# Kernel tuning notes

Measured on AMD Instinct MI355X. Metric: run time of the kernel, lower is better.

## Reference

```python
import jax, jax.numpy as jnp
import numpy as np

N = 100000
E = 1000000
IN_C, HID, OUT_C = 128, 128, 40
DROPOUT_P = 0.5
BN_EPS = 1e-5


def setup_inputs() -> dict:
    key = jax.random.key(0)
    ks = jax.random.split(key, 10)
    x = jax.random.normal(ks[0], (N, IN_C), dtype=jnp.float32)
    edge_index = jax.random.randint(ks[1], (2, E), 0, N, dtype=jnp.int32)

    def glorot(k, fan_in, fan_out):
        lim = np.sqrt(6.0 / (fan_in + fan_out)).astype(np.float32)
        return jax.random.uniform(k, (fan_in, fan_out), jnp.float32, -lim, lim)

    return {
        "x": x,
        "edge_index": edge_index,
        "W1": glorot(ks[2], IN_C, HID), "b1": jnp.zeros((HID,), jnp.float32),
        "g1": jnp.ones((HID,), jnp.float32), "be1": jnp.zeros((HID,), jnp.float32),
        "W2": glorot(ks[3], HID, HID), "b2": jnp.zeros((HID,), jnp.float32),
        "g2": jnp.ones((HID,), jnp.float32), "be2": jnp.zeros((HID,), jnp.float32),
        "W3": glorot(ks[4], HID, OUT_C), "b3": jnp.zeros((OUT_C,), jnp.float32),
    }


def _deg_inv_sqrt(dst):
    # degree from destination nodes, +1 for the added self loop (PyG gcn_norm)
    deg = jax.ops.segment_sum(jnp.ones((E,), jnp.float32), dst, num_segments=N) + 1.0
    return jax.lax.rsqrt(deg)


def _gcn_conv(h, W, b, src, dst, dinv):
    # h: [N, Cin] -> [N, Cout]; y = D^-1/2 (A + I) D^-1/2 (h W) + b
    hw = h @ W
    norm = dinv[src] * dinv[dst]                      # [E]
    msg = hw[src] * norm[:, None]                     # [E, Cout] gather (memory-bound)
    agg = jax.ops.segment_sum(msg, dst, num_segments=N)
    agg = agg + hw * (dinv * dinv)[:, None]           # self-loop contribution
    return agg + b


def _batchnorm(h, gamma, beta):
    mu = jnp.mean(h, axis=0)
    var = jnp.mean(jnp.square(h - mu), axis=0)        # biased, training mode
    return (h - mu) * jax.lax.rsqrt(var + BN_EPS) * gamma + beta


def _dropout(h, key):
    keep = jax.random.bernoulli(key, 1.0 - DROPOUT_P, h.shape)
    return jnp.where(keep, h / (1.0 - DROPOUT_P), 0.0)


def reference(x, edge_index, W1, b1, g1, be1, W2, b2, g2, be2, W3, b3):
    src, dst = edge_index[0], edge_index[1]
    dinv = _deg_inv_sqrt(dst)
    dk = jax.random.split(jax.random.key(42), 2)

    h = _gcn_conv(x, W1, b1, src, dst, dinv)
    h = _dropout(jax.nn.relu(_batchnorm(h, g1, be1)), dk[0])

    h = _gcn_conv(h, W2, b2, src, dst, dinv)
    h = _dropout(jax.nn.relu(_batchnorm(h, g2, be2)), dk[1])

    h = _gcn_conv(h, W3, b3, src, dst, dinv)
    return jax.nn.log_softmax(h, axis=1)
```

## Files before the change

kernel.cpp:

```cpp
#include <hip/hip_runtime.h>
#include <math.h>

typedef __attribute__((ext_vector_type(8))) short bf16x8;
typedef __attribute__((ext_vector_type(4))) float f32x4;

__device__ __forceinline__ float bfbits2f(unsigned short b){
  return __uint_as_float(((unsigned)b) << 16);
}
__device__ __forceinline__ unsigned short f2bfbits(float f){
  unsigned u = __float_as_uint(f);
  unsigned r = u + 0x7fffu + ((u >> 16) & 1u);
  return (unsigned short)(r >> 16);
}

__host__ __device__ __forceinline__ unsigned rotl32(unsigned v, int d){
  return (v << d) | (v >> (32 - d));
}
__host__ __device__ __forceinline__ void tf2x32(unsigned k0, unsigned k1,
                                                unsigned c0, unsigned c1,
                                                unsigned &o0, unsigned &o1)
{
  unsigned ks2 = k0 ^ k1 ^ 0x1BD11BDAu;
  unsigned x0 = c0 + k0, x1 = c1 + k1;
#define TFR(r) x0 += x1; x1 = rotl32(x1, r); x1 ^= x0;
  TFR(13) TFR(15) TFR(26) TFR(6)
  x0 += k1;  x1 += ks2 + 1u;
  TFR(17) TFR(29) TFR(16) TFR(24)
  x0 += ks2; x1 += k0 + 2u;
  TFR(13) TFR(15) TFR(26) TFR(6)
  x0 += k0;  x1 += k1 + 3u;
  TFR(17) TFR(29) TFR(16) TFR(24)
  x0 += k1;  x1 += ks2 + 4u;
  TFR(13) TFR(15) TFR(26) TFR(6)
  x0 += ks2; x1 += k0 + 5u;
#undef TFR
  o0 = x0; o1 = x1;
}

__device__ __forceinline__ void gen_mask(unsigned* __restrict__ mask,
                                         unsigned mk0, unsigned mk1,
                                         int g, int total, int M)
{
  for (int wi = g; wi < M; wi += total){
    unsigned bits = 0u;
    #pragma unroll 4
    for (int j = 0; j < 32; j++){
      unsigned w0, w1;
      tf2x32(mk0, mk1, 0u, (unsigned)wi * 32u + (unsigned)j, w0, w1);
      bits |= (((w0 ^ w1) >> 31) << j);
    }
    mask[wi] = bits;
  }
}

__global__ __launch_bounds__(256) void k_countpos(const int* __restrict__ dst,
                                                  int* __restrict__ cnt,
                                                  int* __restrict__ pos, int E)
{
  int g = blockIdx.x * 256 + threadIdx.x;
  int base = g * 4;
  if (base + 3 < E){
    int4 d = ((const int4*)dst)[g];
    int4 p;
    p.x = atomicAdd(&cnt[d.x], 1);
    p.y = atomicAdd(&cnt[d.y], 1);
    p.z = atomicAdd(&cnt[d.z], 1);
    p.w = atomicAdd(&cnt[d.w], 1);
    ((int4*)pos)[g] = p;
  } else {
    for (int j = 0; j < 4; j++){
      int e = base + j;
      if (e < E) pos[e] = atomicAdd(&cnt[dst[e]], 1);
    }
  }
}

__global__ __launch_bounds__(256) void k_blocksum(const int* __restrict__ cnt,
                                                  int* __restrict__ bsum, int N)
{
  __shared__ int sh[256];
  int t = threadIdx.x;
  int base = blockIdx.x * 1024 + t * 4;
  int s = 0;
  #pragma unroll
  for (int j = 0; j < 4; j++){ int i = base + j; if (i < N) s += cnt[i]; }
  sh[t] = s; __syncthreads();
  for (int off = 128; off; off >>= 1){
    if (t < off) sh[t] += sh[t + off];
    __syncthreads();
  }
  if (t == 0) bsum[blockIdx.x] = sh[0];
}

__global__ __launch_bounds__(256) void k_scansums(const int* __restrict__ bsum,
                                                  int* __restrict__ boff,
                                                  int* __restrict__ rowstart,
                                                  int NB, int N)
{
  __shared__ int sh[256];
  int t = threadIdx.x;
  int v = (t < NB) ? bsum[t] : 0;
  sh[t] = v; __syncthreads();
  for (int off = 1; off < 256; off <<= 1){
    int x = sh[t];
    int y = (t >= off) ? sh[t - off] : 0;
    __syncthreads();
    sh[t] = x + y;
    __syncthreads();
  }
  if (t < NB) boff[t] = sh[t] - v;
  if (t == NB - 1) rowstart[N] = sh[t];
}

__global__ __launch_bounds__(256) void k_scanfinal(const int* __restrict__ cnt,
                                                   const int* __restrict__ boff,
                                                   int* __restrict__ rowstart,
                                                   float* __restrict__ dinv, int N)
{
  __shared__ int sh[256];
  int t = threadIdx.x;
  int base = blockIdx.x * 1024 + t * 4;
  int c0 = 0, c1 = 0, c2 = 0, c3 = 0;
  if (base + 0 < N) c0 = cnt[base + 0];
  if (base + 1 < N) c1 = cnt[base + 1];
  if (base + 2 < N) c2 = cnt[base + 2];
  if (base + 3 < N) c3 = cnt[base + 3];
  int s = c0 + c1 + c2 + c3;
  sh[t] = s; __syncthreads();
  for (int off = 1; off < 256; off <<= 1){
    int x = sh[t];
    int y = (t >= off) ? sh[t - off] : 0;
    __syncthreads();
    sh[t] = x + y;
    __syncthreads();
  }
  int excl = sh[t] - s + boff[blockIdx.x];
  if (base + 0 < N){ rowstart[base+0] = excl;          dinv[base+0] = rsqrtf((float)c0 + 1.f); }
  if (base + 1 < N){ rowstart[base+1] = excl+c0;       dinv[base+1] = rsqrtf((float)c1 + 1.f); }
  if (base + 2 < N){ rowstart[base+2] = excl+c0+c1;    dinv[base+2] = rsqrtf((float)c2 + 1.f); }
  if (base + 3 < N){ rowstart[base+3] = excl+c0+c1+c2; dinv[base+3] = rsqrtf((float)c3 + 1.f); }
}

__global__ __launch_bounds__(256) void k_fill(const int* __restrict__ src,
                                              const int* __restrict__ dst,
                                              const int* __restrict__ pos,
                                              const int* __restrict__ rowstart,
                                              int* __restrict__ csr, int E)
{
  int g = blockIdx.x * 256 + threadIdx.x;
  int base = g * 4;
  if (base + 3 < E){
    int4 d = ((const int4*)dst)[g];
    int4 p = ((const int4*)pos)[g];
    int4 s = ((const int4*)src)[g];
    int r0 = rowstart[d.x], r1 = rowstart[d.y], r2 = rowstart[d.z], r3 = rowstart[d.w];
    csr[r0 + p.x] = s.x;
    csr[r1 + p.y] = s.y;
    csr[r2 + p.z] = s.z;
    csr[r3 + p.w] = s.w;
  } else {
    for (int j = 0; j < 4; j++){
      int e = base + j;
      if (e < E) csr[rowstart[dst[e]] + pos[e]] = src[e];
    }
  }
}

__global__ __launch_bounds__(256) void k_wt(const float* __restrict__ W1,
                                            const float* __restrict__ W2,
                                            const float* __restrict__ W3,
                                            unsigned short* __restrict__ WT1,
                                            unsigned short* __restrict__ WT2,
                                            unsigned short* __restrict__ WT3)
{
  const float* W; unsigned short* WT; int Cout, Cpad;
  if (blockIdx.x == 0){ W = W1; WT = WT1; Cout = 128; Cpad = 128; }
  else if (blockIdx.x == 1){ W = W2; WT = WT2; Cout = 128; Cpad = 128; }
  else { W = W3; WT = WT3; Cout = 40; Cpad = 48; }
  int tot = Cpad * 128;
  for (int i = threadIdx.x; i < tot; i += 256){
    int n = i >> 7, k = i & 127;
    float v = (n < Cout) ? W[k * Cout + n] : 0.f;
    WT[i] = f2bfbits(v);
  }
}

template<int NT, int MODE>
__global__ __launch_bounds__(256) void k_gemm_mfma(const void* __restrict__ Ap,
                                                   const unsigned short* __restrict__ WT,
                                                   const float* __restrict__ dinv,
                                                   const float* __restrict__ stats,
                                                   const float* __restrict__ g,
                                                   const float* __restrict__ be,
                                                   const unsigned* __restrict__ mask,
                                                   float invN,
                                                   unsigned short* __restrict__ outb,
                                                   int N, int Cout)
{
  __shared__ uint4 Wl4[NT * 16 * 16];
  __shared__ uint4 Al4[64 * 16];
  __shared__ float bnS[128], bnB[128];
  const int t = threadIdx.x;
  const int w = t >> 6, l = t & 63;
  const long rb0 = (long)blockIdx.x * 64;
  const int wrow0 = w * 16;

  uint4 rawU[4];
  float4 rawF[4][2];
  unsigned mword[4];
  int rr[4], cc[4];
  bool inr[4];
  #pragma unroll
  for (int i = 0; i < 4; i++){
    int idx = i * 64 + l;
    int r = idx >> 4, c = idx & 15;
    long grow = rb0 + wrow0 + r;
    rr[i] = r; cc[i] = c; inr[i] = (grow < N);
    if (inr[i]){
      if (MODE == 0){
        const float* ap = (const float*)Ap + grow * 128 + c * 8;
        rawF[i][0] = *(const float4*)ap;
        rawF[i][1] = *(const float4*)(ap + 4);
      } else {
        rawU[i] = *(const uint4*)((const unsigned short*)Ap + grow * 128 + c * 8);
        mword[i] = mask[((unsigned)grow << 2) + (c >> 2)];
      }
    }
  }

  {
    const uint4* s4 = (const uint4*)WT;
    const int tot = NT * 16 * 16;
    for (int i = t; i < tot; i += 256){
      int n = i >> 4, c = i & 15;
      Wl4[n * 16 + (c ^ (n & 15))] = s4[i];
    }
  }
  if (MODE == 2 && t < 128){
    float ss = 0.f, qq = 0.f;
    #pragma unroll
    for (int i = 0; i < 16; i++){
      ss += stats[i * 256 + t];
      qq += stats[i * 256 + 128 + t];
    }
    float mean = ss * invN;
    float var = fmaxf(qq * invN - mean * mean, 0.f);
    float rstd = rsqrtf(var + 1e-5f);
    float sc = g[t] * rstd;
    bnS[t] = sc;
    bnB[t] = be[t] - mean * sc;
  }
  __syncthreads();

  #pragma unroll
  for (int i = 0; i < 4; i++){
    uint4 chunk = make_uint4(0u, 0u, 0u, 0u);
    if (inr[i]){
      if (MODE == 0){
        chunk.x = (unsigned)f2bfbits(rawF[i][0].x) | ((unsigned)f2bfbits(rawF[i][0].y) << 16);
        chunk.y = (unsigned)f2bfbits(rawF[i][0].z) | ((unsigned)f2bfbits(rawF[i][0].w) << 16);
        chunk.z = (unsigned)f2bfbits(rawF[i][1].x) | ((unsigned)f2bfbits(rawF[i][1].y) << 16);
        chunk.w = (unsigned)f2bfbits(rawF[i][1].z) | ((unsigned)f2bfbits(rawF[i][1].w) << 16);
      } else {
        unsigned mb = mword[i] >> ((cc[i] & 3) * 8);
        const unsigned* rw = &rawU[i].x;
        unsigned* cw = &chunk.x;
        #pragma unroll
        for (int h = 0; h < 4; h++){
          int ch = cc[i] * 8 + 2 * h;
          float f0 = bfbits2f((unsigned short)(rw[h] & 0xffffu));
          float f1 = bfbits2f((unsigned short)(rw[h] >> 16));
          f0 = fmaxf(fmaf(f0, bnS[ch],     bnB[ch]),     0.f);
          f1 = fmaxf(fmaf(f1, bnS[ch + 1], bnB[ch + 1]), 0.f);
          f0 = ((mb >> (2 * h))     & 1u) ? 0.f : f0 * 2.f;
          f1 = ((mb >> (2 * h + 1)) & 1u) ? 0.f : f1 * 2.f;
          cw[h] = (unsigned)f2bfbits(f0) | ((unsigned)f2bfbits(f1) << 16);
        }
      }
    }
    Al4[(wrow0 + rr[i]) * 16 + (cc[i] ^ rr[i])] = chunk;
  }

  const int lm = l & 15, q = l >> 4;

  f32x4 acc[NT];
  #pragma unroll
  for (int nt = 0; nt < NT; nt++){
    acc[nt][0] = 0.f; acc[nt][1] = 0.f; acc[nt][2] = 0.f; acc[nt][3] = 0.f;
  }

  #pragma unroll
  for (int kt = 0; kt < 4; kt++){
    const int x = kt * 4 + q;
    bf16x8 a = *(const bf16x8*)&Al4[(wrow0 + lm) * 16 + (x ^ lm)];
    #pragma unroll
    for (int nt = 0; nt < NT; nt++){
      int brow = nt * 16 + lm;
      bf16x8 b = *(const bf16x8*)&Wl4[brow * 16 + (x ^ (brow & 15))];
      acc[nt] = __builtin_amdgcn_mfma_f32_16x16x32_bf16(a, b, acc[nt], 0, 0, 0);
    }
  }

  #pragma unroll
  for (int r = 0; r < 4; r++){
    long row = rb0 + wrow0 + q * 4 + r;
    if (row < N){
      float dv = dinv[row];
      #pragma unroll
      for (int nt = 0; nt < NT; nt++){
        int col = nt * 16 + lm;
        if (col < Cout)
          outb[row * Cout + col] = f2bfbits(acc[nt][r] * dv);
      }
    }
  }
}

#define ACC8(U) do{ uint4 _u = (U); \
  a0 += bfbits2f((unsigned short)(_u.x & 0xffffu)); \
  a1 += bfbits2f((unsigned short)(_u.x >> 16)); \
  a2 += bfbits2f((unsigned short)(_u.y & 0xffffu)); \
  a3 += bfbits2f((unsigned short)(_u.y >> 16)); \
  a4 += bfbits2f((unsigned short)(_u.z & 0xffffu)); \
  a5 += bfbits2f((unsigned short)(_u.z >> 16)); \
  a6 += bfbits2f((unsigned short)(_u.w & 0xffffu)); \
  a7 += bfbits2f((unsigned short)(_u.w >> 16)); }while(0)

__global__ __launch_bounds__(256) void k_agg128s(const unsigned short* __restrict__ hw,
                                                 const int* __restrict__ rs,
                                                 const int* __restrict__ csr,
                                                 const float* __restrict__ dinv,
                                                 unsigned short* __restrict__ outb,
                                                 float* __restrict__ stats,
                                                 unsigned* __restrict__ mask,
                                                 unsigned mk0, unsigned mk1, int M,
                                                 int N)
{
  const int l = threadIdx.x;
  const int ns = l >> 4;
  const int sl = l & 15;
  const int ty = threadIdx.y;
  const int grp = ty * 4 + ns;
  const uint4* h16 = (const uint4*)hw;
  const int base = blockIdx.x * 32;

  gen_mask(mask, mk0, mk1, blockIdx.x * 256 + ty * 64 + l, gridDim.x * 256, M);

  float s0=0.f,s1=0.f,s2=0.f,s3=0.f,s4=0.f,s5=0.f,s6=0.f,s7=0.f;
  float q0=0.f,q1=0.f,q2=0.f,q3=0.f,q4=0.f,q5=0.f,q6=0.f,q7=0.f;

  #pragma unroll 1
  for (int it = 0; it < 2; it++){
    int v = base + it * 16 + grp;
    if (v < N){
      float a0=0.f,a1=0.f,a2=0.f,a3=0.f,a4=0.f,a5=0.f,a6=0.f,a7=0.f;
      ACC8(h16[(size_t)v * 16 + sl]);
      int e0 = rs[v], e1 = rs[v + 1];
      int i = e0;
      for (; i + 4 <= e1; i += 4){
        int sa = csr[i], sb = csr[i+1], sc = csr[i+2], sd = csr[i+3];
        uint4 m0 = h16[(size_t)sa * 16 + sl];
        uint4 m1 = h16[(size_t)sb * 16 + sl];
        uint4 m2 = h16[(size_t)sc * 16 + sl];
        uint4 m3 = h16[(size_t)sd * 16 + sl];
        ACC8(m0); ACC8(m1); ACC8(m2); ACC8(m3);
      }
      for (; i < e1; i++){
        ACC8(h16[(size_t)csr[i] * 16 + sl]);
      }
      float dv = dinv[v];
      a0*=dv; a1*=dv; a2*=dv; a3*=dv; a4*=dv; a5*=dv; a6*=dv; a7*=dv;
      uint4 o;
      o.x = (unsigned)f2bfbits(a0) | ((unsigned)f2bfbits(a1) << 16);
      o.y = (unsigned)f2bfbits(a2) | ((unsigned)f2bfbits(a3) << 16);
      o.z = (unsigned)f2bfbits(a4) | ((unsigned)f2bfbits(a5) << 16);
      o.w = (unsigned)f2bfbits(a6) | ((unsigned)f2bfbits(a7) << 16);
      ((uint4*)outb)[(size_t)v * 16 + sl] = o;
      s0+=a0; q0=fmaf(a0,a0,q0);  s1+=a1; q1=fmaf(a1,a1,q1);
      s2+=a2; q2=fmaf(a2,a2,q2);  s3+=a3; q3=fmaf(a3,a3,q3);
      s4+=a4; q4=fmaf(a4,a4,q4);  s5+=a5; q5=fmaf(a5,a5,q5);
      s6+=a6; q6=fmaf(a6,a6,q6);  s7+=a7; q7=fmaf(a7,a7,q7);
    }
  }

  __shared__ float shS[16][128], shQ[16][128];
  *(float4*)&shS[grp][sl * 8]     = make_float4(s0, s1, s2, s3);
  *(float4*)&shS[grp][sl * 8 + 4] = make_float4(s4, s5, s6, s7);
  *(float4*)&shQ[grp][sl * 8]     = make_float4(q0, q1, q2, q3);
  *(float4*)&shQ[grp][sl * 8 + 4] = make_float4(q4, q5, q6, q7);
  __syncthreads();
  int t = ty * 64 + threadIdx.x;
  if (t < 128){
    float ss = 0.f, qq = 0.f;
    #pragma unroll
    for (int g2 = 0; g2 < 16; g2++){ ss += shS[g2][t]; qq += shQ[g2][t]; }
    float* dstat = stats + (blockIdx.x & 15) * 256;
    atomicAdd(&dstat[t], ss);
    atomicAdd(&dstat[128 + t], qq);
  }
}

__global__ __launch_bounds__(256) void k_agg40lsm(const unsigned short* __restrict__ hw,
                                                  const int* __restrict__ rs,
                                                  const int* __restrict__ csr,
                                                  const float* __restrict__ dinv,
                                                  const float* __restrict__ b3,
                                                  float* __restrict__ out, int N)
{
  const int l = threadIdx.x;
  const int ns = l >> 4, sl = l & 15;
  const int v = blockIdx.x * 16 + threadIdx.y * 4 + ns;
  const bool act = (v < N) && (sl < 10);
  const uint2* h2 = (const uint2*)hw;
  float a0 = 0.f, a1 = 0.f, a2 = 0.f, a3 = 0.f, dv = 1.f;
  if (act){
    dv = dinv[v];
    uint2 u = h2[(size_t)v * 10 + sl];
    a0 = bfbits2f((unsigned short)(u.x & 0xffffu));
    a1 = bfbits2f((unsigned short)(u.x >> 16));
    a2 = bfbits2f((unsigned short)(u.y & 0xffffu));
    a3 = bfbits2f((unsigned short)(u.y >> 16));
    int e0 = rs[v], e1 = rs[v + 1];
    int i = e0;
#define ACCU2(U) do{ uint2 _u = (U); \
    a0 += bfbits2f((unsigned short)(_u.x & 0xffffu)); \
    a1 += bfbits2f((unsigned short)(_u.x >> 16)); \
    a2 += bfbits2f((unsigned short)(_u.y & 0xffffu)); \
    a3 += bfbits2f((unsigned short)(_u.y >> 16)); }while(0)
    for (; i + 4 <= e1; i += 4){
      int sa = csr[i], sb = csr[i+1], sc = csr[i+2], sd = csr[i+3];
      uint2 m0 = h2[(size_t)sa * 10 + sl];
      uint2 m1 = h2[(size_t)sb * 10 + sl];
      uint2 m2 = h2[(size_t)sc * 10 + sl];
      uint2 m3 = h2[(size_t)sd * 10 + sl];
      ACCU2(m0); ACCU2(m1); ACCU2(m2); ACCU2(m3);
    }
    for (; i < e1; i++){
      ACCU2(h2[(size_t)csr[i] * 10 + sl]);
    }
#undef ACCU2
  }
  float x0 = act ? fmaf(a0, dv, b3[sl * 4 + 0]) : -INFINITY;
  float x1 = act ? fmaf(a1, dv, b3[sl * 4 + 1]) : -INFINITY;
  float x2 = act ? fmaf(a2, dv, b3[sl * 4 + 2]) : -INFINITY;
  float x3 = act ? fmaf(a3, dv, b3[sl * 4 + 3]) : -INFINITY;
  float m = fmaxf(fmaxf(x0, x1), fmaxf(x2, x3));
  #pragma unroll
  for (int off = 8; off; off >>= 1) m = fmaxf(m, __shfl_xor(m, off, 16));
  float e = act ? (expf(x0 - m) + expf(x1 - m) + expf(x2 - m) + expf(x3 - m)) : 0.f;
  #pragma unroll
  for (int off = 8; off; off >>= 1) e += __shfl_xor(e, off, 16);
  float lse = m + logf(e);
  if (act){
    float4 o;
    o.x = x0 - lse; o.y = x1 - lse; o.z = x2 - lse; o.w = x3 - lse;
    *reinterpret_cast<float4*>(out + (size_t)v * 40 + sl * 4) = o;
  }
}

extern "C" void kernel_launch(void* const* d_in, const int* in_sizes, int n_in,
                              void* d_out, int out_size, void* d_ws, size_t ws_size,
                              hipStream_t stream)
{
  const float* x  = (const float*)d_in[0];
  const int* ei   = (const int*)d_in[1];
  const float* W1 = (const float*)d_in[2];
  const float* g1 = (const float*)d_in[4];
  const float* be1= (const float*)d_in[5];
  const float* W2 = (const float*)d_in[6];
  const float* g2 = (const float*)d_in[8];
  const float* be2= (const float*)d_in[9];
  const float* W3 = (const float*)d_in[10];
  const float* b3 = (const float*)d_in[11];
  float* out = (float*)d_out;

  const int N = in_sizes[0] / 128;
  const int E = in_sizes[1] / 2;
  const int* srcv = ei;
  const int* dstv = ei + E;

  char* ws = (char*)d_ws;
  size_t off = 0;
  auto take = [&](size_t bytes) -> void* {
    void* p = ws + off;
    off = (off + bytes + 255) & ~(size_t)255;
    return p;
  };
  int*   cnt      = (int*)  take((size_t)N * 4);
  int*   pos      = (int*)  take((size_t)E * 4);
  int*   rowstart = (int*)  take((size_t)(N + 1) * 4);
  int*   csr      = (int*)  take((size_t)E * 4);
  float* dinv     = (float*)take((size_t)N * 4);
  int*   bsum     = (int*)  take(256 * 4);
  int*   boff     = (int*)  take(256 * 4);
  float* stats1   = (float*)take(2 * 16 * 256 * 4);
  float* stats2   = stats1 + 16 * 256;
  unsigned* mask1 = (unsigned*)take((size_t)N * 4 * 4);
  unsigned* mask2 = (unsigned*)take((size_t)N * 4 * 4);
  unsigned short* WT1 = (unsigned short*)take(128 * 128 * 2);
  unsigned short* WT2 = (unsigned short*)take(128 * 128 * 2);
  unsigned short* WT3 = (unsigned short*)take(48 * 128 * 2);
  unsigned short* bufX = (unsigned short*)take((size_t)N * 128 * 2);
  unsigned short* bufY = (unsigned short*)take((size_t)N * 128 * 2);
  (void)ws_size; (void)n_in; (void)out_size;

  unsigned l1k0, l1k1, l2k0, l2k1;
  tf2x32(0u, 42u, 0u, 0u, l1k0, l1k1);
  tf2x32(0u, 42u, 0u, 1u, l2k0, l2k1);

  const float invN = 1.0f / (float)N;
  const int M = N * 4;
  const int NB = (N + 1023) / 1024;
  dim3 wblk(64, 4);
  dim3 wgrid16((N + 15) / 16);
  dim3 wgrid32((N + 31) / 32);
  const int ggrid = (N + 63) / 64;
  const int egrid = (E + 1023) / 1024;

  hipMemsetAsync(cnt, 0, (size_t)N * 4, stream);
  hipMemsetAsync(stats1, 0, 2 * 16 * 256 * 4, stream);
  k_countpos<<<egrid, 256, 0, stream>>>(dstv, cnt, pos, E);
  k_blocksum<<<NB, 256, 0, stream>>>(cnt, bsum, N);
  k_scansums<<<1, 256, 0, stream>>>(bsum, boff, rowstart, NB, N);
  k_scanfinal<<<NB, 256, 0, stream>>>(cnt, boff, rowstart, dinv, N);
  k_fill<<<egrid, 256, 0, stream>>>(srcv, dstv, pos, rowstart, csr, E);
  k_wt<<<3, 256, 0, stream>>>(W1, W2, W3, WT1, WT2, WT3);

  k_gemm_mfma<8, 0><<<ggrid, 256, 0, stream>>>(x, WT1, dinv,
      nullptr, nullptr, nullptr, nullptr, invN, bufX, N, 128);
  k_agg128s<<<wgrid32, wblk, 0, stream>>>(bufX, rowstart, csr, dinv, bufY, stats1,
      mask1, l1k0, l1k1, M, N);

  k_gemm_mfma<8, 2><<<ggrid, 256, 0, stream>>>(bufY, WT2, dinv,
      stats1, g1, be1, mask1, invN, bufX, N, 128);
  k_agg128s<<<wgrid32, wblk, 0, stream>>>(bufX, rowstart, csr, dinv, bufY, stats2,
      mask2, l2k0, l2k1, M, N);

  k_gemm_mfma<3, 2><<<ggrid, 256, 0, stream>>>(bufY, WT3, dinv,
      stats2, g2, be2, mask2, invN, bufX, N, 40);
  k_agg40lsm<<<wgrid16, wblk, 0, stream>>>(bufX, rowstart, csr, dinv, b3, out, N);
}
```

Baseline: 404.9 us.

## Move dropout mask generation into CSR build kernels and pad layer-3 rows

Dropout mask generation (Threefry hashing) moves out of the aggregation kernels and into the countpos and fill kernels of the CSR build, so the gather-heavy aggregations no longer carry that ALU work. Gathers now use 32-bit byte offsets instead of 64-bit index arithmetic. The layer-3 GEMM output gets a row stride of 64, so each 40-wide row starts at a 128-byte boundary. The 40-wide aggregation also reads rows at a 128-byte stride, so the two stay consistent. Risk: the build kernels get heavier, and the unsigned offsets overflow only for very large N.

Result: no change. 409.4 us (+1.1%).

```diff
diff --git a/kernel.cpp b/kernel.cpp
--- a/kernel.cpp
+++ b/kernel.cpp
@@ -11,6 +11,13 @@
   unsigned u = __float_as_uint(f);
   unsigned r = u + 0x7fffu + ((u >> 16) & 1u);
   return (unsigned short)(r >> 16);
+}
+
+__device__ __forceinline__ uint4 ld16(const void* __restrict__ base, unsigned byteoff){
+  return *(const uint4*)((const char*)base + byteoff);
+}
+__device__ __forceinline__ uint2 ld8(const void* __restrict__ base, unsigned byteoff){
+  return *(const uint2*)((const char*)base + byteoff);
 }
 
 __host__ __device__ __forceinline__ unsigned rotl32(unsigned v, int d){
@@ -55,7 +62,9 @@
 
 __global__ __launch_bounds__(256) void k_countpos(const int* __restrict__ dst,
                                                   int* __restrict__ cnt,
-                                                  int* __restrict__ pos, int E)
+                                                  int* __restrict__ pos, int E,
+                                                  unsigned* __restrict__ mask,
+                                                  unsigned mk0, unsigned mk1, int M)
 {
   int g = blockIdx.x * 256 + threadIdx.x;
   int base = g * 4;
@@ -66,12 +75,14 @@
     p.y = atomicAdd(&cnt[d.y], 1);
     p.z = atomicAdd(&cnt[d.z], 1);
     p.w = atomicAdd(&cnt[d.w], 1);
+    gen_mask(mask, mk0, mk1, g, gridDim.x * 256, M);
     ((int4*)pos)[g] = p;
   } else {
     for (int j = 0; j < 4; j++){
       int e = base + j;
       if (e < E) pos[e] = atomicAdd(&cnt[dst[e]], 1);
     }
+    gen_mask(mask, mk0, mk1, g, gridDim.x * 256, M);
   }
 }
 
@@ -145,7 +156,9 @@
                                               const int* __restrict__ dst,
                                               const int* __restrict__ pos,
                                               const int* __restrict__ rowstart,
-                                              int* __restrict__ csr, int E)
+                                              int* __restrict__ csr, int E,
+                                              unsigned* __restrict__ mask,
+                                              unsigned mk0, unsigned mk1, int M)
 {
   int g = blockIdx.x * 256 + threadIdx.x;
   int base = g * 4;
@@ -164,6 +177,7 @@
       if (e < E) csr[rowstart[dst[e]] + pos[e]] = src[e];
     }
   }
+  gen_mask(mask, mk0, mk1, g, gridDim.x * 256, M);
 }
 
 __global__ __launch_bounds__(256) void k_wt(const float* __restrict__ W1,
@@ -195,7 +209,7 @@
                                                    const unsigned* __restrict__ mask,
                                                    float invN,
                                                    unsigned short* __restrict__ outb,
-                                                   int N, int Cout)
+                                                   int N, int Cout, int Cstride)
 {
   __shared__ uint4 Wl4[NT * 16 * 16];
   __shared__ uint4 Al4[64 * 16];
@@ -310,7 +324,7 @@
       for (int nt = 0; nt < NT; nt++){
         int col = nt * 16 + lm;
         if (col < Cout)
-          outb[row * Cout + col] = f2bfbits(acc[nt][r] * dv);
+          outb[row * Cstride + col] = f2bfbits(acc[nt][r] * dv);
       }
     }
   }
@@ -332,8 +346,6 @@
                                                  const float* __restrict__ dinv,
                                                  unsigned short* __restrict__ outb,
                                                  float* __restrict__ stats,
-                                                 unsigned* __restrict__ mask,
-                                                 unsigned mk0, unsigned mk1, int M,
                                                  int N)
 {
   const int l = threadIdx.x;
@@ -341,10 +353,8 @@
   const int sl = l & 15;
   const int ty = threadIdx.y;
   const int grp = ty * 4 + ns;
-  const uint4* h16 = (const uint4*)hw;
   const int base = blockIdx.x * 32;
-
-  gen_mask(mask, mk0, mk1, blockIdx.x * 256 + ty * 64 + l, gridDim.x * 256, M);
+  const unsigned slB = (unsigned)sl * 16u;
 
   float s0=0.f,s1=0.f,s2=0.f,s3=0.f,s4=0.f,s5=0.f,s6=0.f,s7=0.f;
   float q0=0.f,q1=0.f,q2=0.f,q3=0.f,q4=0.f,q5=0.f,q6=0.f,q7=0.f;
@@ -354,19 +364,19 @@
     int v = base + it * 16 + grp;
     if (v < N){
       float a0=0.f,a1=0.f,a2=0.f,a3=0.f,a4=0.f,a5=0.f,a6=0.f,a7=0.f;
-      ACC8(h16[(size_t)v * 16 + sl]);
+      ACC8(ld16(hw, (unsigned)v * 256u + slB));
       int e0 = rs[v], e1 = rs[v + 1];
       int i = e0;
       for (; i + 4 <= e1; i += 4){
         int sa = csr[i], sb = csr[i+1], sc = csr[i+2], sd = csr[i+3];
-        uint4 m0 = h16[(size_t)sa * 16 + sl];
-        uint4 m1 = h16[(size_t)sb * 16 + sl];
-        uint4 m2 = h16[(size_t)sc * 16 + sl];
-        uint4 m3 = h16[(size_t)sd * 16 + sl];
+        uint4 m0 = ld16(hw, (unsigned)sa * 256u + slB);
+        uint4 m1 = ld16(hw, (unsigned)sb * 256u + slB);
+        uint4 m2 = ld16(hw, (unsigned)sc * 256u + slB);
+        uint4 m3 = ld16(hw, (unsigned)sd * 256u + slB);
         ACC8(m0); ACC8(m1); ACC8(m2); ACC8(m3);
       }
       for (; i < e1; i++){
-        ACC8(h16[(size_t)csr[i] * 16 + sl]);
+        ACC8(ld16(hw, (unsigned)csr[i] * 256u + slB));
       }
       float dv = dinv[v];
       a0*=dv; a1*=dv; a2*=dv; a3*=dv; a4*=dv; a5*=dv; a6*=dv; a7*=dv;
@@ -375,7 +385,7 @@
       o.y = (unsigned)f2bfbits(a2) | ((unsigned)f2bfbits(a3) << 16);
       o.z = (unsigned)f2bfbits(a4) | ((unsigned)f2bfbits(a5) << 16);
       o.w = (unsigned)f2bfbits(a6) | ((unsigned)f2bfbits(a7) << 16);
-      ((uint4*)outb)[(size_t)v * 16 + sl] = o;
+      *(uint4*)((char*)outb + (unsigned)v * 256u + slB) = o;
       s0+=a0; q0=fmaf(a0,a0,q0);  s1+=a1; q1=fmaf(a1,a1,q1);
       s2+=a2; q2=fmaf(a2,a2,q2);  s3+=a3; q3=fmaf(a3,a3,q3);
       s4+=a4; q4=fmaf(a4,a4,q4);  s5+=a5; q5=fmaf(a5,a5,q5);
@@ -411,11 +421,11 @@
   const int ns = l >> 4, sl = l & 15;
   const int v = blockIdx.x * 16 + threadIdx.y * 4 + ns;
   const bool act = (v < N) && (sl < 10);
-  const uint2* h2 = (const uint2*)hw;
+  const unsigned slB = (unsigned)sl * 8u;
   float a0 = 0.f, a1 = 0.f, a2 = 0.f, a3 = 0.f, dv = 1.f;
   if (act){
     dv = dinv[v];
-    uint2 u = h2[(size_t)v * 10 + sl];
+    uint2 u = ld8(hw, (unsigned)v * 128u + slB);
     a0 = bfbits2f((unsigned short)(u.x & 0xffffu));
     a1 = bfbits2f((unsigned short)(u.x >> 16));
     a2 = bfbits2f((unsigned short)(u.y & 0xffffu));
@@ -429,14 +439,14 @@
     a3 += bfbits2f((unsigned short)(_u.y >> 16)); }while(0)
     for (; i + 4 <= e1; i += 4){
       int sa = csr[i], sb = csr[i+1], sc = csr[i+2], sd = csr[i+3];
-      uint2 m0 = h2[(size_t)sa * 10 + sl];
-      uint2 m1 = h2[(size_t)sb * 10 + sl];
-      uint2 m2 = h2[(size_t)sc * 10 + sl];
-      uint2 m3 = h2[(size_t)sd * 10 + sl];
+      uint2 m0 = ld8(hw, (unsigned)sa * 128u + slB);
+      uint2 m1 = ld8(hw, (unsigned)sb * 128u + slB);
+      uint2 m2 = ld8(hw, (unsigned)sc * 128u + slB);
+      uint2 m3 = ld8(hw, (unsigned)sd * 128u + slB);
       ACCU2(m0); ACCU2(m1); ACCU2(m2); ACCU2(m3);
     }
     for (; i < e1; i++){
-      ACCU2(h2[(size_t)csr[i] * 10 + sl]);
+      ACCU2(ld8(hw, (unsigned)csr[i] * 128u + slB));
     }
 #undef ACCU2
   }
@@ -519,24 +529,22 @@
 
   hipMemsetAsync(cnt, 0, (size_t)N * 4, stream);
   hipMemsetAsync(stats1, 0, 2 * 16 * 256 * 4, stream);
-  k_countpos<<<egrid, 256, 0, stream>>>(dstv, cnt, pos, E);
+  k_countpos<<<egrid, 256, 0, stream>>>(dstv, cnt, pos, E, mask1, l1k0, l1k1, M);
   k_blocksum<<<NB, 256, 0, stream>>>(cnt, bsum, N);
   k_scansums<<<1, 256, 0, stream>>>(bsum, boff, rowstart, NB, N);
   k_scanfinal<<<NB, 256, 0, stream>>>(cnt, boff, rowstart, dinv, N);
-  k_fill<<<egrid, 256, 0, stream>>>(srcv, dstv, pos, rowstart, csr, E);
+  k_fill<<<egrid, 256, 0, stream>>>(srcv, dstv, pos, rowstart, csr, E, mask2, l2k0, l2k1, M);
   k_wt<<<3, 256, 0, stream>>>(W1, W2, W3, WT1, WT2, WT3);
 
   k_gemm_mfma<8, 0><<<ggrid, 256, 0, stream>>>(x, WT1, dinv,
-      nullptr, nullptr, nullptr, nullptr, invN, bufX, N, 128);
-  k_agg128s<<<wgrid32, wblk, 0, stream>>>(bufX, rowstart, csr, dinv, bufY, stats1,
-      mask1, l1k0, l1k1, M, N);
+      nullptr, nullptr, nullptr, nullptr, invN, bufX, N, 128, 128);
+  k_agg128s<<<wgrid32, wblk, 0, stream>>>(bufX, rowstart, csr, dinv, bufY, stats1, N);
 
   k_gemm_mfma<8, 2><<<ggrid, 256, 0, stream>>>(bufY, WT2, dinv,
-      stats1, g1, be1, mask1, invN, bufX, N, 128);
-  k_agg128s<<<wgrid32, wblk, 0, stream>>>(bufX, rowstart, csr, dinv, bufY, stats2,
-      mask2, l2k0, l2k1, M, N);
+      stats1, g1, be1, mask1, invN, bufX, N, 128, 128);
+  k_agg128s<<<wgrid32, wblk, 0, stream>>>(bufX, rowstart, csr, dinv, bufY, stats2, N);
 
   k_gemm_mfma<3, 2><<<ggrid, 256, 0, stream>>>(bufY, WT3, dinv,
-      stats2, g2, be2, mask2, invN, bufX, N, 40);
+      stats2, g2, be2, mask2, invN, bufX, N, 40, 64);
   k_agg40lsm<<<wgrid16, wblk, 0, stream>>>(bufX, rowstart, csr, dinv, b3, out, N);
 }
```
